# Optimization experiments

Measured on AMD Instinct MI355X. Metric: run time of the kernel, lower is better.

The kernel has to match this reference:

```python
import jax, jax.numpy as jnp
import numpy as np

N_NODES = 100000
N_EDGES = 1600000
IN_DIM, HIDDEN, OUT = 256, 128, 64


def setup_inputs() -> dict:
    key = jax.random.key(0)
    k1, k2, k3, k4 = jax.random.split(key, 4)
    x = jax.random.normal(k1, (N_NODES, IN_DIM), dtype=jnp.float32)
    edge_index = jax.random.randint(k2, (2, N_EDGES), 0, N_NODES, dtype=jnp.int32)
    # glorot-ish init for the GCN linear layers
    W1 = jax.random.normal(k3, (IN_DIM, HIDDEN), dtype=jnp.float32) / np.sqrt(IN_DIM)
    b1 = jnp.zeros((HIDDEN,), dtype=jnp.float32)
    W2 = jax.random.normal(k4, (HIDDEN, OUT), dtype=jnp.float32) / np.sqrt(HIDDEN)
    b2 = jnp.zeros((OUT,), dtype=jnp.float32)
    return {"x": x, "edge_index": edge_index, "W1": W1, "b1": b1, "W2": W2, "b2": b2}


def gcn_layer(x, src, dst, W, b):
    """PyG GCNConv: add self-loops, symmetric deg^-1/2 normalization,
    linear transform, scatter-add aggregation, bias."""
    h = x @ W  # [N, F_out]
    # degree over self-looped graph: in-degree(dst counts) + 1 self loop
    deg = jax.ops.segment_sum(jnp.ones((src.shape[0],), h.dtype), dst,
                              num_segments=N_NODES) + 1.0
    dinv = jax.lax.rsqrt(deg)  # [N]
    coef = dinv[src] * dinv[dst]  # [E]
    agg = jax.ops.segment_sum(h[src] * coef[:, None], dst, num_segments=N_NODES)
    # self-loop contribution (norm = dinv[i]^2) without materializing loop edges
    agg = agg + h * (dinv * dinv)[:, None]
    return agg + b


def reference(x, edge_index, W1, b1, W2, b2):
    src, dst = edge_index[0], edge_index[1]
    h = jax.nn.relu(gcn_layer(x, src, dst, W1, b1))
    return jax.nn.relu(gcn_layer(h, src, dst, W2, b2))
```

## Files before the change

kernel.cpp:

```cpp
#include <hip/hip_runtime.h>

#define N_NODES 100000
#define N_EDGES 1600000
#define IN_DIM 256
#define HIDDEN 128
#define OUT_DIM 64

#define NBIN 391
#define NBLK3 256
#define CHUNK 6250
#define NMAT (NBIN * NBLK3)
#define NBLK_SCAN (NMAT / 256)
#define CAP 6144

#define LDK1 264
#define LDK2 136

typedef __bf16 bf16x8 __attribute__((ext_vector_type(8)));
typedef __bf16 bf16x4 __attribute__((ext_vector_type(4)));
typedef float f32x4 __attribute__((ext_vector_type(4)));

__launch_bounds__(256)
__global__ void k_hist(const int* __restrict__ dst, int* __restrict__ cnt2) {
    __shared__ int hist[NBIN];
    for (int i = threadIdx.x; i < NBIN; i += 256) hist[i] = 0;
    __syncthreads();
    int base = blockIdx.x * CHUNK;
    for (int i = threadIdx.x; i < CHUNK; i += 256)
        atomicAdd(&hist[dst[base + i] >> 8], 1);
    __syncthreads();
    for (int k = threadIdx.x; k < NBIN; k += 256)
        cnt2[k * NBLK3 + blockIdx.x] = hist[k];
}

__global__ void k_scan1(int* __restrict__ a, int* __restrict__ bsum) {
    __shared__ int tmp[256];
    int t = threadIdx.x;
    int i = blockIdx.x * 256 + t;
    int v = a[i];
    tmp[t] = v;
    __syncthreads();
    #pragma unroll
    for (int off = 1; off < 256; off <<= 1) {
        int p = (t >= off) ? tmp[t - off] : 0;
        __syncthreads();
        tmp[t] += p;
        __syncthreads();
    }
    a[i] = tmp[t] - v;
    if (t == 255) bsum[blockIdx.x] = tmp[255];
}

__global__ void k_scan2(int* __restrict__ bsum) {
    __shared__ int tmp[512];
    int t = threadIdx.x;
    int v = (t < NBLK_SCAN) ? bsum[t] : 0;
    tmp[t] = v;
    __syncthreads();
    #pragma unroll
    for (int off = 1; off < 512; off <<= 1) {
        int p = (t >= off) ? tmp[t - off] : 0;
        __syncthreads();
        tmp[t] += p;
        __syncthreads();
    }
    if (t < NBLK_SCAN) bsum[t] = tmp[t] - v;
}

__global__ void k_scan3(int* __restrict__ a, const int* __restrict__ bsum) {
    int i = blockIdx.x * 256 + threadIdx.x;
    a[i] += bsum[blockIdx.x];
}

__launch_bounds__(256)
__global__ void k_scatter_bins(const int* __restrict__ src, const int* __restrict__ dst,
                               const int* __restrict__ off2,
                               unsigned int* __restrict__ ebuf) {
    __shared__ int cursor[NBIN];
    for (int k = threadIdx.x; k < NBIN; k += 256)
        cursor[k] = off2[k * NBLK3 + blockIdx.x];
    __syncthreads();
    int base = blockIdx.x * CHUNK;
    for (int i = threadIdx.x; i < CHUNK; i += 256) {
        int s = src[base + i], d = dst[base + i];
        int pos = atomicAdd(&cursor[d >> 8], 1);
        ebuf[pos] = ((unsigned)s << 8) | (unsigned)(d & 255);
    }
}

__launch_bounds__(256)
__global__ void k_fine(const unsigned int* __restrict__ ebuf, const int* __restrict__ off2,
                       int* __restrict__ esrc, int* __restrict__ rowstart,
                       float* __restrict__ dinv) {
    __shared__ int hist[256];
    __shared__ int tmp[256];
    __shared__ int nodeoff[256];
    __shared__ int cursor[256];
    __shared__ unsigned int ed[CAP];
    __shared__ int sOut[CAP];

    const int k = blockIdx.x;
    const int t = threadIdx.x;
    const int e0 = off2[k * NBLK3];
    const int e1 = (k + 1 < NBIN) ? off2[(k + 1) * NBLK3] : N_EDGES;
    int m = e1 - e0;
    if (m > CAP) m = CAP;

    hist[t] = 0;
    __syncthreads();
    for (int i = t; i < m; i += 256) {
        unsigned v = ebuf[e0 + i];
        ed[i] = v;
        atomicAdd(&hist[v & 255], 1);
    }
    __syncthreads();

    int v = hist[t];
    tmp[t] = v;
    __syncthreads();
    #pragma unroll
    for (int off = 1; off < 256; off <<= 1) {
        int p = (t >= off) ? tmp[t - off] : 0;
        __syncthreads();
        tmp[t] += p;
        __syncthreads();
    }
    nodeoff[t] = tmp[t] - v;
    cursor[t] = tmp[t] - v;
    __syncthreads();

    for (int i = t; i < m; i += 256) {
        unsigned e = ed[i];
        int pos = atomicAdd(&cursor[e & 255], 1);
        sOut[pos] = (int)(e >> 8);
    }
    __syncthreads();

    for (int i = t; i < m; i += 256) esrc[e0 + i] = sOut[i];

    int n = k * 256 + t;
    if (n < N_NODES) {
        rowstart[n] = e0 + nodeoff[t];
        dinv[n] = rsqrtf((float)hist[t] + 1.0f);
    }
    if (k == 0 && t == 0) rowstart[N_NODES] = N_EDGES;
}

__launch_bounds__(256, 2)
__global__ void k_gemm1(const float* __restrict__ X, const float* __restrict__ W1,
                        __bf16* __restrict__ H) {
    __shared__ __attribute__((aligned(16))) __bf16 Bs[HIDDEN * LDK1];

    const int t = threadIdx.x;
    const int wave = t >> 6;
    const int lane = t & 63;
    const int wr = wave >> 1, wc = wave & 1;
    const int lm = lane & 15;
    const int q = lane >> 4;
    const int row0 = blockIdx.x * 128 + wr * 64;
    const int colbase = wc * 64;

    #pragma unroll
    for (int it = 0; it < 16; ++it) {
        int idx = it * 256 + t;
        int k2 = idx >> 5;
        int c = (idx & 31) * 4;
        float4 v0 = *(const float4*)&W1[(2 * k2) * HIDDEN + c];
        float4 v1 = *(const float4*)&W1[(2 * k2 + 1) * HIDDEN + c];
        const float lo[4] = {v0.x, v0.y, v0.z, v0.w};
        const float hi[4] = {v1.x, v1.y, v1.z, v1.w};
        #pragma unroll
        for (int i = 0; i < 4; ++i) {
            __bf16 pair[2] = {(__bf16)lo[i], (__bf16)hi[i]};
            *(unsigned int*)&Bs[(c + i) * LDK1 + 2 * k2] = *(unsigned int*)pair;
        }
    }
    __syncthreads();

    const float* xp[4];
    #pragma unroll
    for (int mi = 0; mi < 4; ++mi) {
        int r = row0 + mi * 16 + lm;
        if (r > N_NODES - 1) r = N_NODES - 1;
        xp[mi] = &X[r * IN_DIM];
    }

    f32x4 acc[4][4] = {};

    #pragma unroll
    for (int ks = 0; ks < 8; ++ks) {
        bf16x8 af[4];
        #pragma unroll
        for (int mi = 0; mi < 4; ++mi) {
            float4 a0 = *(const float4*)&xp[mi][ks * 32 + q * 8];
            float4 a1 = *(const float4*)&xp[mi][ks * 32 + q * 8 + 4];
            bf16x8 f;
            f[0] = (__bf16)a0.x; f[1] = (__bf16)a0.y;
            f[2] = (__bf16)a0.z; f[3] = (__bf16)a0.w;
            f[4] = (__bf16)a1.x; f[5] = (__bf16)a1.y;
            f[6] = (__bf16)a1.z; f[7] = (__bf16)a1.w;
            af[mi] = f;
        }
        bf16x8 bfr[4];
        #pragma unroll
        for (int ni = 0; ni < 4; ++ni)
            bfr[ni] = *(const bf16x8*)&Bs[(colbase + ni * 16 + lm) * LDK1 + ks * 32 + q * 8];
        #pragma unroll
        for (int mi = 0; mi < 4; ++mi)
            #pragma unroll
            for (int ni = 0; ni < 4; ++ni)
                acc[mi][ni] = __builtin_amdgcn_mfma_f32_16x16x32_bf16(
                    af[mi], bfr[ni], acc[mi][ni], 0, 0, 0);
    }

    #pragma unroll
    for (int mi = 0; mi < 4; ++mi) {
        #pragma unroll
        for (int r = 0; r < 4; ++r) {
            int grow = row0 + mi * 16 + q * 4 + r;
            if (grow < N_NODES) {
                #pragma unroll
                for (int ni = 0; ni < 4; ++ni)
                    H[grow * HIDDEN + colbase + ni * 16 + lm] = (__bf16)acc[mi][ni][r];
            }
        }
    }
}

__launch_bounds__(256)
__global__ void k_gather1(const int* __restrict__ rowstart, const int* __restrict__ esrc,
                          const float* __restrict__ dinv,
                          const __bf16* __restrict__ H, const float* __restrict__ b1,
                          __bf16* __restrict__ AGG) {
    int n = blockIdx.x * 16 + (threadIdx.x >> 4);
    if (n >= N_NODES) return;
    int j = (threadIdx.x & 15) * 8;

    float dn = dinv[n];
    float s = dn * dn;
    bf16x8 h = *(const bf16x8*)&H[n * HIDDEN + j];
    float acc[8];
    #pragma unroll
    for (int i = 0; i < 8; ++i) acc[i] = (float)h[i] * s;

    int p0 = rowstart[n], p1 = rowstart[n + 1];
    int p = p0;
    for (; p + 3 < p1; p += 4) {
        int s0 = esrc[p + 0], s1 = esrc[p + 1], s2 = esrc[p + 2], s3 = esrc[p + 3];
        float c0 = dinv[s0] * dn, c1 = dinv[s1] * dn;
        float c2 = dinv[s2] * dn, c3 = dinv[s3] * dn;
        bf16x8 v0 = *(const bf16x8*)&H[s0 * HIDDEN + j];
        bf16x8 v1 = *(const bf16x8*)&H[s1 * HIDDEN + j];
        bf16x8 v2 = *(const bf16x8*)&H[s2 * HIDDEN + j];
        bf16x8 v3 = *(const bf16x8*)&H[s3 * HIDDEN + j];
        #pragma unroll
        for (int i = 0; i < 8; ++i) acc[i] = fmaf((float)v0[i], c0, acc[i]);
        #pragma unroll
        for (int i = 0; i < 8; ++i) acc[i] = fmaf((float)v1[i], c1, acc[i]);
        #pragma unroll
        for (int i = 0; i < 8; ++i) acc[i] = fmaf((float)v2[i], c2, acc[i]);
        #pragma unroll
        for (int i = 0; i < 8; ++i) acc[i] = fmaf((float)v3[i], c3, acc[i]);
    }
    for (; p < p1; ++p) {
        int sidx = esrc[p];
        float c = dinv[sidx] * dn;
        bf16x8 v = *(const bf16x8*)&H[sidx * HIDDEN + j];
        #pragma unroll
        for (int i = 0; i < 8; ++i) acc[i] = fmaf((float)v[i], c, acc[i]);
    }

    float4 bb0 = *(const float4*)&b1[j];
    float4 bb1 = *(const float4*)&b1[j + 4];
    bf16x8 o;
    o[0] = (__bf16)fmaxf(acc[0] + bb0.x, 0.f);
    o[1] = (__bf16)fmaxf(acc[1] + bb0.y, 0.f);
    o[2] = (__bf16)fmaxf(acc[2] + bb0.z, 0.f);
    o[3] = (__bf16)fmaxf(acc[3] + bb0.w, 0.f);
    o[4] = (__bf16)fmaxf(acc[4] + bb1.x, 0.f);
    o[5] = (__bf16)fmaxf(acc[5] + bb1.y, 0.f);
    o[6] = (__bf16)fmaxf(acc[6] + bb1.z, 0.f);
    o[7] = (__bf16)fmaxf(acc[7] + bb1.w, 0.f);
    *(bf16x8*)&AGG[n * HIDDEN + j] = o;
}

__launch_bounds__(256, 2)
__global__ void k_gemm2(const __bf16* __restrict__ AGG, const float* __restrict__ W2,
                        __bf16* __restrict__ H2) {
    __shared__ __attribute__((aligned(16))) __bf16 Bs[OUT_DIM * LDK2];

    const int t = threadIdx.x;
    const int wave = t >> 6;
    const int lane = t & 63;
    const int lm = lane & 15;
    const int q = lane >> 4;
    const int row0 = blockIdx.x * 256 + wave * 64;

    #pragma unroll
    for (int it = 0; it < 4; ++it) {
        int idx = it * 256 + t;
        int k2 = idx >> 4;
        int c = (idx & 15) * 4;
        float4 v0 = *(const float4*)&W2[(2 * k2) * OUT_DIM + c];
        float4 v1 = *(const float4*)&W2[(2 * k2 + 1) * OUT_DIM + c];
        const float lo[4] = {v0.x, v0.y, v0.z, v0.w};
        const float hi[4] = {v1.x, v1.y, v1.z, v1.w};
        #pragma unroll
        for (int i = 0; i < 4; ++i) {
            __bf16 pair[2] = {(__bf16)lo[i], (__bf16)hi[i]};
            *(unsigned int*)&Bs[(c + i) * LDK2 + 2 * k2] = *(unsigned int*)pair;
        }
    }
    __syncthreads();

    const __bf16* ap[4];
    #pragma unroll
    for (int mi = 0; mi < 4; ++mi) {
        int r = row0 + mi * 16 + lm;
        if (r > N_NODES - 1) r = N_NODES - 1;
        ap[mi] = &AGG[r * HIDDEN];
    }

    f32x4 acc[4][4] = {};

    #pragma unroll
    for (int ks = 0; ks < 4; ++ks) {
        bf16x8 af[4];
        #pragma unroll
        for (int mi = 0; mi < 4; ++mi)
            af[mi] = *(const bf16x8*)&ap[mi][ks * 32 + q * 8];
        bf16x8 bfr[4];
        #pragma unroll
        for (int ni = 0; ni < 4; ++ni)
            bfr[ni] = *(const bf16x8*)&Bs[(ni * 16 + lm) * LDK2 + ks * 32 + q * 8];
        #pragma unroll
        for (int mi = 0; mi < 4; ++mi)
            #pragma unroll
            for (int ni = 0; ni < 4; ++ni)
                acc[mi][ni] = __builtin_amdgcn_mfma_f32_16x16x32_bf16(
                    af[mi], bfr[ni], acc[mi][ni], 0, 0, 0);
    }

    #pragma unroll
    for (int mi = 0; mi < 4; ++mi) {
        #pragma unroll
        for (int r = 0; r < 4; ++r) {
            int grow = row0 + mi * 16 + q * 4 + r;
            if (grow < N_NODES) {
                #pragma unroll
                for (int ni = 0; ni < 4; ++ni)
                    H2[grow * OUT_DIM + ni * 16 + lm] = (__bf16)acc[mi][ni][r];
            }
        }
    }
}

__launch_bounds__(256)
__global__ void k_gather2(const int* __restrict__ rowstart, const int* __restrict__ esrc,
                          const float* __restrict__ dinv,
                          const __bf16* __restrict__ H2, const float* __restrict__ b2,
                          float* __restrict__ OUT) {
    int n = blockIdx.x * 32 + (threadIdx.x >> 3);
    if (n >= N_NODES) return;
    int j = (threadIdx.x & 7) * 8;

    float dn = dinv[n];
    float s = dn * dn;
    bf16x8 h = *(const bf16x8*)&H2[n * OUT_DIM + j];
    float acc[8];
    #pragma unroll
    for (int i = 0; i < 8; ++i) acc[i] = (float)h[i] * s;

    int p0 = rowstart[n], p1 = rowstart[n + 1];
    int p = p0;
    for (; p + 3 < p1; p += 4) {
        int s0 = esrc[p + 0], s1 = esrc[p + 1], s2 = esrc[p + 2], s3 = esrc[p + 3];
        float c0 = dinv[s0] * dn, c1 = dinv[s1] * dn;
        float c2 = dinv[s2] * dn, c3 = dinv[s3] * dn;
        bf16x8 v0 = *(const bf16x8*)&H2[s0 * OUT_DIM + j];
        bf16x8 v1 = *(const bf16x8*)&H2[s1 * OUT_DIM + j];
        bf16x8 v2 = *(const bf16x8*)&H2[s2 * OUT_DIM + j];
        bf16x8 v3 = *(const bf16x8*)&H2[s3 * OUT_DIM + j];
        #pragma unroll
        for (int i = 0; i < 8; ++i) acc[i] = fmaf((float)v0[i], c0, acc[i]);
        #pragma unroll
        for (int i = 0; i < 8; ++i) acc[i] = fmaf((float)v1[i], c1, acc[i]);
        #pragma unroll
        for (int i = 0; i < 8; ++i) acc[i] = fmaf((float)v2[i], c2, acc[i]);
        #pragma unroll
        for (int i = 0; i < 8; ++i) acc[i] = fmaf((float)v3[i], c3, acc[i]);
    }
    for (; p < p1; ++p) {
        int sidx = esrc[p];
        float c = dinv[sidx] * dn;
        bf16x8 v = *(const bf16x8*)&H2[sidx * OUT_DIM + j];
        #pragma unroll
        for (int i = 0; i < 8; ++i) acc[i] = fmaf((float)v[i], c, acc[i]);
    }

    float4 bb0 = *(const float4*)&b2[j];
    float4 bb1 = *(const float4*)&b2[j + 4];
    float4 o0, o1;
    o0.x = fmaxf(acc[0] + bb0.x, 0.f);
    o0.y = fmaxf(acc[1] + bb0.y, 0.f);
    o0.z = fmaxf(acc[2] + bb0.z, 0.f);
    o0.w = fmaxf(acc[3] + bb0.w, 0.f);
    o1.x = fmaxf(acc[4] + bb1.x, 0.f);
    o1.y = fmaxf(acc[5] + bb1.y, 0.f);
    o1.z = fmaxf(acc[6] + bb1.z, 0.f);
    o1.w = fmaxf(acc[7] + bb1.w, 0.f);
    *(float4*)&OUT[n * OUT_DIM + j] = o0;
    *(float4*)&OUT[n * OUT_DIM + j + 4] = o1;
}

extern "C" void kernel_launch(void* const* d_in, const int* in_sizes, int n_in,
                              void* d_out, int out_size, void* d_ws, size_t ws_size,
                              hipStream_t stream) {
    const float* x  = (const float*)d_in[0];
    const int* ei   = (const int*)d_in[1];
    const float* W1 = (const float*)d_in[2];
    const float* b1 = (const float*)d_in[3];
    const float* W2 = (const float*)d_in[4];
    const float* b2 = (const float*)d_in[5];
    float* out = (float*)d_out;

    const int* src = ei;
    const int* dst = ei + N_EDGES;

    char* ws = (char*)d_ws;
    int*          cnt2     = (int*)         (ws + 0x000000);
    int*          bsum     = (int*)         (ws + 0x080000);
    int*          rowstart = (int*)         (ws + 0x090000);
    float*        dinv     = (float*)       (ws + 0x100000);
    unsigned int* ebuf     = (unsigned int*)(ws + 0x180000);
    int*          esrc     = (int*)         (ws + 0x800000);
    __bf16*       h1       = (__bf16*)      (ws + 0xE80000);
    __bf16*       agg1     = (__bf16*)      (ws + 0x2880000);
    __bf16*       h2       = (__bf16*)      (ws + 0x4280000);

    k_hist<<<NBLK3, 256, 0, stream>>>(dst, cnt2);
    k_scan1<<<NBLK_SCAN, 256, 0, stream>>>(cnt2, bsum);
    k_scan2<<<1, 512, 0, stream>>>(bsum);
    k_scan3<<<NBLK_SCAN, 256, 0, stream>>>(cnt2, bsum);
    k_scatter_bins<<<NBLK3, 256, 0, stream>>>(src, dst, cnt2, ebuf);
    k_fine<<<NBIN, 256, 0, stream>>>(ebuf, cnt2, esrc, rowstart, dinv);

    k_gemm1<<<(N_NODES + 127) / 128, 256, 0, stream>>>(x, W1, h1);
    k_gather1<<<(N_NODES + 15) / 16, 256, 0, stream>>>(rowstart, esrc, dinv, h1, b1, agg1);
    k_gemm2<<<(N_NODES + 255) / 256, 256, 0, stream>>>(agg1, W2, h2);
    k_gather2<<<(N_NODES + 31) / 32, 256, 0, stream>>>(rowstart, esrc, dinv, h2, b2, out);
}
```

Baseline: 356.2 us.

## Pre-transpose weights once and stage activation tiles through LDS in GEMMs

Adds a small prep kernel that transposes W1 and W2 into bf16 K-major buffers, so each GEMM block no longer converts and transposes the full weight matrix into shared memory. The GEMMs now stage coalesced row-major activation chunks into a padded LDS tile and read B fragments straight from global memory (L2-resident). The aim is to cut per-block weight setup and the uncoalesced per-lane activation loads. The cost is an extra launch, extra syncthreads per K chunk, and B fragments coming from global memory instead of LDS.

```diff
diff --git a/kernel.cpp b/kernel.cpp
--- a/kernel.cpp
+++ b/kernel.cpp
@@ -12,9 +12,6 @@
 #define NMAT (NBIN * NBLK3)
 #define NBLK_SCAN (NMAT / 256)
 #define CAP 6144
-
-#define LDK1 264
-#define LDK2 136
 
 typedef __bf16 bf16x8 __attribute__((ext_vector_type(8)));
 typedef __bf16 bf16x4 __attribute__((ext_vector_type(4)));
@@ -146,10 +143,32 @@
     if (k == 0 && t == 0) rowstart[N_NODES] = N_EDGES;
 }
 
+__launch_bounds__(256)
+__global__ void k_prep(const float* __restrict__ W1, const float* __restrict__ W2,
+                       __bf16* __restrict__ w1t, __bf16* __restrict__ w2t) {
+    __shared__ float tile[32][33];
+    int b = blockIdx.x;
+    const float* W; __bf16* WT; int ldw, ldt, k0, n0;
+    if (b < 32) { W = W1; WT = w1t; ldw = HIDDEN; ldt = IN_DIM;
+                  k0 = (b >> 2) * 32; n0 = (b & 3) * 32; }
+    else { b -= 32; W = W2; WT = w2t; ldw = OUT_DIM; ldt = HIDDEN;
+           k0 = (b >> 1) * 32; n0 = (b & 1) * 32; }
+    int t = threadIdx.x;
+    int r = t >> 3, c4 = (t & 7) * 4;
+    float4 v = *(const float4*)&W[(k0 + r) * ldw + n0 + c4];
+    tile[r][c4 + 0] = v.x; tile[r][c4 + 1] = v.y;
+    tile[r][c4 + 2] = v.z; tile[r][c4 + 3] = v.w;
+    __syncthreads();
+    bf16x4 o;
+    o[0] = (__bf16)tile[c4 + 0][r]; o[1] = (__bf16)tile[c4 + 1][r];
+    o[2] = (__bf16)tile[c4 + 2][r]; o[3] = (__bf16)tile[c4 + 3][r];
+    *(bf16x4*)&WT[(n0 + r) * ldt + k0 + c4] = o;
+}
+
 __launch_bounds__(256, 2)
-__global__ void k_gemm1(const float* __restrict__ X, const float* __restrict__ W1,
+__global__ void k_gemm1(const float* __restrict__ X, const __bf16* __restrict__ w1t,
                         __bf16* __restrict__ H) {
-    __shared__ __attribute__((aligned(16))) __bf16 Bs[HIDDEN * LDK1];
+    __shared__ __attribute__((aligned(16))) __bf16 As[128 * 17 * 8];
 
     const int t = threadIdx.x;
     const int wave = t >> 6;
@@ -157,67 +176,60 @@
     const int wr = wave >> 1, wc = wave & 1;
     const int lm = lane & 15;
     const int q = lane >> 4;
-    const int row0 = blockIdx.x * 128 + wr * 64;
+    const int row0 = blockIdx.x * 128;
     const int colbase = wc * 64;
 
-    #pragma unroll
-    for (int it = 0; it < 16; ++it) {
-        int idx = it * 256 + t;
-        int k2 = idx >> 5;
-        int c = (idx & 31) * 4;
-        float4 v0 = *(const float4*)&W1[(2 * k2) * HIDDEN + c];
-        float4 v1 = *(const float4*)&W1[(2 * k2 + 1) * HIDDEN + c];
-        const float lo[4] = {v0.x, v0.y, v0.z, v0.w};
-        const float hi[4] = {v1.x, v1.y, v1.z, v1.w};
-        #pragma unroll
-        for (int i = 0; i < 4; ++i) {
-            __bf16 pair[2] = {(__bf16)lo[i], (__bf16)hi[i]};
-            *(unsigned int*)&Bs[(c + i) * LDK1 + 2 * k2] = *(unsigned int*)pair;
-        }
-    }
-    __syncthreads();
-
-    const float* xp[4];
-    #pragma unroll
-    for (int mi = 0; mi < 4; ++mi) {
-        int r = row0 + mi * 16 + lm;
-        if (r > N_NODES - 1) r = N_NODES - 1;
-        xp[mi] = &X[r * IN_DIM];
-    }
-
     f32x4 acc[4][4] = {};
 
     #pragma unroll
-    for (int ks = 0; ks < 8; ++ks) {
-        bf16x8 af[4];
-        #pragma unroll
-        for (int mi = 0; mi < 4; ++mi) {
-            float4 a0 = *(const float4*)&xp[mi][ks * 32 + q * 8];
-            float4 a1 = *(const float4*)&xp[mi][ks * 32 + q * 8 + 4];
+    for (int chunk = 0; chunk < 2; ++chunk) {
+        const int k0 = chunk * 128;
+        #pragma unroll
+        for (int it = 0; it < 8; ++it) {
+            int row = it * 16 + (t >> 4);
+            int kc = t & 15;
+            int grow = row0 + row;
+            if (grow > N_NODES - 1) grow = N_NODES - 1;
+            const float* xr = &X[grow * IN_DIM + k0 + kc * 8];
+            float4 a0 = *(const float4*)&xr[0];
+            float4 a1 = *(const float4*)&xr[4];
             bf16x8 f;
             f[0] = (__bf16)a0.x; f[1] = (__bf16)a0.y;
             f[2] = (__bf16)a0.z; f[3] = (__bf16)a0.w;
             f[4] = (__bf16)a1.x; f[5] = (__bf16)a1.y;
             f[6] = (__bf16)a1.z; f[7] = (__bf16)a1.w;
-            af[mi] = f;
-        }
-        bf16x8 bfr[4];
-        #pragma unroll
-        for (int ni = 0; ni < 4; ++ni)
-            bfr[ni] = *(const bf16x8*)&Bs[(colbase + ni * 16 + lm) * LDK1 + ks * 32 + q * 8];
-        #pragma unroll
-        for (int mi = 0; mi < 4; ++mi)
+            int g = it * 16 + kc;
+            *(bf16x8*)&As[(g * 17 + (t >> 4)) * 8] = f;
+        }
+        __syncthreads();
+
+        #pragma unroll
+        for (int ks = 0; ks < 4; ++ks) {
+            bf16x8 af[4], bfr[4];
+            #pragma unroll
+            for (int mi = 0; mi < 4; ++mi) {
+                int g = (wr * 4 + mi) * 16 + ks * 4 + q;
+                af[mi] = *(const bf16x8*)&As[(g * 17 + lm) * 8];
+            }
             #pragma unroll
             for (int ni = 0; ni < 4; ++ni)
-                acc[mi][ni] = __builtin_amdgcn_mfma_f32_16x16x32_bf16(
-                    af[mi], bfr[ni], acc[mi][ni], 0, 0, 0);
+                bfr[ni] = *(const bf16x8*)
+                    &w1t[(colbase + ni * 16 + lm) * IN_DIM + k0 + ks * 32 + q * 8];
+            #pragma unroll
+            for (int mi = 0; mi < 4; ++mi)
+                #pragma unroll
+                for (int ni = 0; ni < 4; ++ni)
+                    acc[mi][ni] = __builtin_amdgcn_mfma_f32_16x16x32_bf16(
+                        af[mi], bfr[ni], acc[mi][ni], 0, 0, 0);
+        }
+        __syncthreads();
     }
 
     #pragma unroll
     for (int mi = 0; mi < 4; ++mi) {
         #pragma unroll
         for (int r = 0; r < 4; ++r) {
-            int grow = row0 + mi * 16 + q * 4 + r;
+            int grow = row0 + wr * 64 + mi * 16 + q * 4 + r;
             if (grow < N_NODES) {
                 #pragma unroll
                 for (int ni = 0; ni < 4; ++ni)
@@ -285,67 +297,61 @@
 }
 
 __launch_bounds__(256, 2)
-__global__ void k_gemm2(const __bf16* __restrict__ AGG, const float* __restrict__ W2,
+__global__ void k_gemm2(const __bf16* __restrict__ AGG, const __bf16* __restrict__ w2t,
                         __bf16* __restrict__ H2) {
-    __shared__ __attribute__((aligned(16))) __bf16 Bs[OUT_DIM * LDK2];
+    __shared__ __attribute__((aligned(16))) __bf16 As[128 * 17 * 8];
 
     const int t = threadIdx.x;
     const int wave = t >> 6;
     const int lane = t & 63;
     const int lm = lane & 15;
     const int q = lane >> 4;
-    const int row0 = blockIdx.x * 256 + wave * 64;
-
-    #pragma unroll
-    for (int it = 0; it < 4; ++it) {
-        int idx = it * 256 + t;
-        int k2 = idx >> 4;
-        int c = (idx & 15) * 4;
-        float4 v0 = *(const float4*)&W2[(2 * k2) * OUT_DIM + c];
-        float4 v1 = *(const float4*)&W2[(2 * k2 + 1) * OUT_DIM + c];
-        const float lo[4] = {v0.x, v0.y, v0.z, v0.w};
-        const float hi[4] = {v1.x, v1.y, v1.z, v1.w};
-        #pragma unroll
-        for (int i = 0; i < 4; ++i) {
-            __bf16 pair[2] = {(__bf16)lo[i], (__bf16)hi[i]};
-            *(unsigned int*)&Bs[(c + i) * LDK2 + 2 * k2] = *(unsigned int*)pair;
-        }
-    }
-    __syncthreads();
-
-    const __bf16* ap[4];
+    const int row0 = blockIdx.x * 256;
+
+    f32x4 acc[4][4] = {};
+
+    #pragma unroll
+    for (int chunk = 0; chunk < 2; ++chunk) {
+        const int k0 = chunk * 64;
+        #pragma unroll
+        for (int it = 0; it < 8; ++it) {
+            int row = it * 32 + (t >> 3);
+            int kc = t & 7;
+            int grow = row0 + row;
+            if (grow > N_NODES - 1) grow = N_NODES - 1;
+            bf16x8 f = *(const bf16x8*)&AGG[grow * HIDDEN + k0 + kc * 8];
+            int g = (row >> 4) * 8 + kc;
+            *(bf16x8*)&As[(g * 17 + (row & 15)) * 8] = f;
+        }
+        __syncthreads();
+
+        #pragma unroll
+        for (int ks = 0; ks < 2; ++ks) {
+            bf16x8 af[4], bfr[4];
+            #pragma unroll
+            for (int mi = 0; mi < 4; ++mi) {
+                int g = (wave * 4 + mi) * 8 + ks * 4 + q;
+                af[mi] = *(const bf16x8*)&As[(g * 17 + lm) * 8];
+            }
+            #pragma unroll
+            for (int ni = 0; ni < 4; ++ni)
+                bfr[ni] = *(const bf16x8*)
+                    &w2t[(ni * 16 + lm) * HIDDEN + k0 + ks * 32 + q * 8];
+            #pragma unroll
+            for (int mi = 0; mi < 4; ++mi)
+                #pragma unroll
+                for (int ni = 0; ni < 4; ++ni)
+                    acc[mi][ni] = __builtin_amdgcn_mfma_f32_16x16x32_bf16(
+                        af[mi], bfr[ni], acc[mi][ni], 0, 0, 0);
+        }
+        __syncthreads();
+    }
+
     #pragma unroll
     for (int mi = 0; mi < 4; ++mi) {
-        int r = row0 + mi * 16 + lm;
-        if (r > N_NODES - 1) r = N_NODES - 1;
-        ap[mi] = &AGG[r * HIDDEN];
-    }
-
-    f32x4 acc[4][4] = {};
-
-    #pragma unroll
-    for (int ks = 0; ks < 4; ++ks) {
-        bf16x8 af[4];
-        #pragma unroll
-        for (int mi = 0; mi < 4; ++mi)
-            af[mi] = *(const bf16x8*)&ap[mi][ks * 32 + q * 8];
-        bf16x8 bfr[4];
-        #pragma unroll
-        for (int ni = 0; ni < 4; ++ni)
-            bfr[ni] = *(const bf16x8*)&Bs[(ni * 16 + lm) * LDK2 + ks * 32 + q * 8];
-        #pragma unroll
-        for (int mi = 0; mi < 4; ++mi)
-            #pragma unroll
-            for (int ni = 0; ni < 4; ++ni)
-                acc[mi][ni] = __builtin_amdgcn_mfma_f32_16x16x32_bf16(
-                    af[mi], bfr[ni], acc[mi][ni], 0, 0, 0);
-    }
-
-    #pragma unroll
-    for (int mi = 0; mi < 4; ++mi) {
         #pragma unroll
         for (int r = 0; r < 4; ++r) {
-            int grow = row0 + mi * 16 + q * 4 + r;
+            int grow = row0 + wave * 64 + mi * 16 + q * 4 + r;
             if (grow < N_NODES) {
                 #pragma unroll
                 for (int ni = 0; ni < 4; ++ni)
@@ -437,7 +443,10 @@
     __bf16*       h1       = (__bf16*)      (ws + 0xE80000);
     __bf16*       agg1     = (__bf16*)      (ws + 0x2880000);
     __bf16*       h2       = (__bf16*)      (ws + 0x4280000);
-
+    __bf16*       w1t      = (__bf16*)      (ws + 0x4F00000);
+    __bf16*       w2t      = (__bf16*)      (ws + 0x4F20000);
+
+    k_prep<<<40, 256, 0, stream>>>(W1, W2, w1t, w2t);
     k_hist<<<NBLK3, 256, 0, stream>>>(dst, cnt2);
     k_scan1<<<NBLK_SCAN, 256, 0, stream>>>(cnt2, bsum);
     k_scan2<<<1, 512, 0, stream>>>(bsum);
@@ -445,8 +454,8 @@
     k_scatter_bins<<<NBLK3, 256, 0, stream>>>(src, dst, cnt2, ebuf);
     k_fine<<<NBIN, 256, 0, stream>>>(ebuf, cnt2, esrc, rowstart, dinv);
 
-    k_gemm1<<<(N_NODES + 127) / 128, 256, 0, stream>>>(x, W1, h1);
+    k_gemm1<<<(N_NODES + 127) / 128, 256, 0, stream>>>(x, w1t, h1);
     k_gather1<<<(N_NODES + 15) / 16, 256, 0, stream>>>(rowstart, esrc, dinv, h1, b1, agg1);
-    k_gemm2<<<(N_NODES + 255) / 256, 256, 0, stream>>>(agg1, W2, h2);
+    k_gemm2<<<(N_NODES + 255) / 256, 256, 0, stream>>>(agg1, w2t, h2);
     k_gather2<<<(N_NODES + 31) / 32, 256, 0, stream>>>(rowstart, esrc, dinv, h2, b2, out);
 }
```

Measured after the change: 353.3 us. About the same (-0.8%).
